# Optimization experiments

Hardware: AMD Instinct MI355X
Metric: run time of the kernel (lower is better)

## Reference

```python
import jax, jax.numpy as jnp
import numpy as np
import math

B, T1, T2, T3, D = 8, 32, 32, 16, 512
L, DL = 20, 128


def setup_inputs() -> dict:
    key = jax.random.key(0)
    ks = jax.random.split(key, 16)
    s = lambda fan: 1.0 / math.sqrt(fan)
    return {
        "f_c": jax.random.normal(ks[0], (B, T1, T2, T3, D), jnp.float32),
        "f_w": jax.random.normal(ks[1], (B, L, D), jnp.float32),
        "f_s": jax.random.normal(ks[2], (B, D), jnp.float32),
        "f_m": jax.random.normal(ks[3], (B, T1, T2, D), jnp.float32),
        "Wc_down": jax.random.normal(ks[4], (DL, D), jnp.float32) * s(D),
        "bc_down": jnp.zeros((DL,), jnp.float32),
        "Ww": jax.random.normal(ks[5], (DL, D), jnp.float32) * s(D),
        "bw": jnp.zeros((DL,), jnp.float32),
        "Ws": jax.random.normal(ks[6], (DL, D), jnp.float32) * s(D),
        "bs": jnp.zeros((DL,), jnp.float32),
        "Wq": jax.random.normal(ks[7], (DL, DL), jnp.float32) * s(DL),
        "bq": jnp.zeros((DL,), jnp.float32),
        "Wk": jax.random.normal(ks[8], (DL, DL), jnp.float32) * s(DL),
        "bk": jnp.zeros((DL,), jnp.float32),
        "Wc_up": jax.random.normal(ks[9], (D, DL), jnp.float32) * s(DL),
        "bc_up": jnp.zeros((D,), jnp.float32),
    }


def reference(f_c, f_w, f_s, f_m, Wc_down, bc_down, Ww, bw, Ws, bs,
              Wq, bq, Wk, bk, Wc_up, bc_up):
    inv_sqrt_dl = 1.0 / math.sqrt(DL)
    # 1x1 conv projections == per-position linear layers
    f_c_hat = jnp.einsum('bxyzd,ld->bxyzl', f_c, Wc_down) + bc_down  # [B,T1,T2,T3,dl]
    f_w_hat = f_w @ Ww.T + bw                                        # [B,L,dl]
    f_s_hat = f_s @ Ws.T + bs                                        # [B,dl]
    # Content attention: query from map, key/value from words
    q = f_c_hat @ Wq.T + bq                                          # [B,T1,T2,T3,dl]
    k = f_w_hat @ Wk.T + bk                                          # [B,L,dl]
    scores = jnp.einsum('bxyzd,bld->bxyzl', q, k) * inv_sqrt_dl
    attn = jax.nn.softmax(scores, axis=-1)
    f_caq = jnp.einsum('bxyzl,bld->bxyzd', attn, f_w_hat)            # [B,T1,T2,T3,dl]
    # Gate with sentence feature
    f_cq = f_c_hat * (f_caq + f_s_hat[:, None, None, None, :])
    # Self-attention over last spatial axis (T3)
    A_c = jnp.einsum('bxyzd,bxywd->bxyzw', f_cq, f_cq) * inv_sqrt_dl  # [B,T1,T2,T3,T3]
    A_c = jax.nn.softmax(A_c, axis=-1)
    f_cc_hat = jnp.einsum('bxyzw,bxywd->bxyzd', A_c, f_c_hat)
    f_cc = jnp.einsum('bxyzl,dl->bxyzd', f_cc_hat, Wc_up) + bc_up     # [B,T1,T2,T3,D]
    # Sigmoid gating residual for f_m
    g_m = jax.nn.sigmoid(f_m * f_s[:, None, None, :])
    fbar_m = g_m * f_m                                                # [B,T1,T2,D]
    return f_cc + f_c + fbar_m[:, :, :, None, :]
```

## Files before the change

### kernel.cpp

```cpp
#include <hip/hip_runtime.h>
#include <math.h>

#define B_ 8
#define T1_ 32
#define T2_ 32
#define T3_ 16
#define D_ 512
#define L_ 20
#define DL_ 128
#define M_ (B_*T1_*T2_*T3_)

#define WS_FW   0
#define WS_KQ   20480
#define WS_FS   40960
#define WS_SB   41984
#define WS_WDB  42144
#define WS_WUB  74912

typedef __attribute__((ext_vector_type(8))) short short8_t;
typedef __attribute__((ext_vector_type(4))) float f32x4;

__device__ __forceinline__ unsigned short f2b(float f) {
  unsigned int u = __float_as_uint(f);
  return (unsigned short)((u + 0x7fffu + ((u >> 16) & 1u)) >> 16);
}
__device__ __forceinline__ float b2f(short s) {
  return __uint_as_float(((unsigned)(unsigned short)s) << 16);
}
__device__ __forceinline__ int4 pack8(float4 a, float4 b) {
  int4 p;
  p.x = (int)f2b(a.x) | ((int)f2b(a.y) << 16);
  p.y = (int)f2b(a.z) | ((int)f2b(a.w) << 16);
  p.z = (int)f2b(b.x) | ((int)f2b(b.y) << 16);
  p.w = (int)f2b(b.z) | ((int)f2b(b.w) << 16);
  return p;
}

__global__ __launch_bounds__(256) void k0_convert(
    const float* __restrict__ Wd, const float* __restrict__ Wu,
    unsigned short* __restrict__ wdb, unsigned short* __restrict__ wub) {
  int g = blockIdx.x * 256 + threadIdx.x;
  if (g < 16384) {
    float4 v = ((const float4*)Wd)[g];
    ushort4 h; h.x = f2b(v.x); h.y = f2b(v.y); h.z = f2b(v.z); h.w = f2b(v.w);
    ((ushort4*)wdb)[g] = h;
  } else {
    int q = g - 16384;
    float4 v = ((const float4*)Wu)[q];
    ushort4 h; h.x = f2b(v.x); h.y = f2b(v.y); h.z = f2b(v.z); h.w = f2b(v.w);
    ((ushort4*)wub)[q] = h;
  }
}

__global__ __launch_bounds__(128) void k1_small(
    const float* __restrict__ f_w, const float* __restrict__ f_s,
    const float* __restrict__ Ww, const float* __restrict__ bw,
    const float* __restrict__ Ws, const float* __restrict__ bs,
    const float* __restrict__ Wq, const float* __restrict__ bq,
    const float* __restrict__ Wk, const float* __restrict__ bk,
    float* __restrict__ ws) {
  const int bl = blockIdx.x;
  const int b = bl / L_, l = bl % L_;
  const int d = threadIdx.x;
  __shared__ float s_fw[DL_];
  __shared__ float s_k[DL_];
  {
    const float* x = f_w + (size_t)(b*L_+l)*D_;
    const float* w = Ww + (size_t)d*D_;
    float acc = 0.f;
    for (int i = 0; i < D_; i += 4)
      acc += x[i]*w[i] + x[i+1]*w[i+1] + x[i+2]*w[i+2] + x[i+3]*w[i+3];
    acc += bw[d];
    s_fw[d] = acc;
    ws[WS_FW + (b*L_+l)*DL_ + d] = acc;
  }
  if (l == 0) {
    const float* x = f_s + (size_t)b*D_;
    const float* w = Ws + (size_t)d*D_;
    float acc = 0.f;
    for (int i = 0; i < D_; i += 4)
      acc += x[i]*w[i] + x[i+1]*w[i+1] + x[i+2]*w[i+2] + x[i+3]*w[i+3];
    ws[WS_FS + b*DL_ + d] = acc + bs[d];
  }
  __syncthreads();
  {
    const float* w = Wk + (size_t)d*DL_;
    float acc = 0.f;
    for (int i = 0; i < DL_; ++i) acc += s_fw[i]*w[i];
    s_k[d] = acc + bk[d];
  }
  __syncthreads();
  {
    float acc = 0.f;
    for (int c = 0; c < DL_; ++c) acc += s_k[c] * Wq[c*DL_ + d];
    ws[WS_KQ + (b*L_+l)*DL_ + d] = acc;
  }
  if (d == 0) {
    float acc = 0.f;
    for (int c = 0; c < DL_; ++c) acc += bq[c]*s_k[c];
    ws[WS_SB + b*L_ + l] = acc;
  }
}

#define SFCH_B 0
#define FCQ_B  8192
#define WD_B   16384
#define FC_B   32768
#define KQ_B   16384
#define FWT_B  24576
#define ATB_B  32768
#define FS_B   36864
#define SB_B   37376
#define ATTN_B 37504
#define AC_B   37504
#define WU_B   16384
#define SMEM_B 40960

__global__ __launch_bounds__(256, 4) void k2_fused(
    const float* __restrict__ f_c, const unsigned short* __restrict__ wdb,
    const unsigned short* __restrict__ wub,
    const float* __restrict__ bc_down, const float* __restrict__ bc_up,
    const float* __restrict__ f_m, const float* __restrict__ f_s,
    const float* __restrict__ ws, float* __restrict__ out) {
  __shared__ __align__(16) char smb[SMEM_B];
  float* sAttn = (float*)(smb + ATTN_B);
  float* sAc   = (float*)(smb + AC_B);
  float* sFs   = (float*)(smb + FS_B);
  float* sSb   = (float*)(smb + SB_B);

  const int t = threadIdx.x;
  const int row0 = blockIdx.x * 32;
  const int b = row0 >> 14;
  const int lane = t & 63, w = t >> 6;
  const int l15 = lane & 15, l4 = lane >> 4;
  const int wr = (w & 1) * 16;
  const int wc = w >> 1;
  const float inv_sqrt_dl = 0.08838834764831843f;
  const f32x4 z4 = {0.f, 0.f, 0.f, 0.f};
  const int sd_r = t >> 3, sd_k8 = (t & 7) * 8;

  f32x4 dacc[4];
  #pragma unroll
  for (int cf = 0; cf < 4; ++cf) dacc[cf] = z4;

  for (int kc = 0; kc < D_; kc += 64) {
    #pragma unroll
    for (int i = 0; i < 4; ++i) {
      int idx = t + i*256;
      int d = idx >> 3, kb = idx & 7;
      *(int4*)(smb + WD_B + d*128 + ((kb*16) ^ ((d & 7) << 4))) =
        *(const int4*)(wdb + (size_t)d*D_ + kc + kb*8);
    }
    {
      const float* src = f_c + (size_t)(row0 + sd_r)*D_ + kc + sd_k8;
      float4 v0 = *(const float4*)src;
      float4 v1 = *(const float4*)(src + 4);
      int4 pk = pack8(v0, v1);
      *(int4*)(smb + FC_B + sd_r*128 + ((sd_k8*2) ^ ((sd_r & 7) << 4))) = pk;
    }
    __syncthreads();
    #pragma unroll
    for (int ks = 0; ks < 2; ++ks) {
      const int rr = wr + l15;
      short8_t bfrag = *(const short8_t*)(smb + FC_B + rr*128 +
                        ((ks*64 + l4*16) ^ ((rr & 7) << 4)));
      #pragma unroll
      for (int cf = 0; cf < 4; ++cf) {
        const int d = wc*64 + cf*16 + l15;
        short8_t afrag = *(const short8_t*)(smb + WD_B + d*128 +
                          ((ks*64 + l4*16) ^ ((d & 7) << 4)));
        dacc[cf] = __builtin_amdgcn_mfma_f32_16x16x32_bf16(afrag, bfrag, dacc[cf], 0, 0, 0);
      }
    }
    __syncthreads();
  }
  {
    const int rr = wr + l15;
    const int rs = (rr & 7) << 4;
    #pragma unroll
    for (int cf = 0; cf < 4; ++cf) {
      const int d0 = wc*64 + cf*16 + l4*4;
      float4 bias = *(const float4*)(bc_down + d0);
      ushort4 pk;
      pk.x = f2b(dacc[cf][0] + bias.x); pk.y = f2b(dacc[cf][1] + bias.y);
      pk.z = f2b(dacc[cf][2] + bias.z); pk.w = f2b(dacc[cf][3] + bias.w);
      *(ushort4*)(smb + SFCH_B + rr*256 + ((d0*2) ^ rs)) = pk;
    }
  }
  for (int p = t; p < 32*16; p += 256) {
    const int l = p >> 4, k8 = (p & 15) * 8;
    int4 v = {0,0,0,0};
    if (l < L_) {
      float4 a0 = *(const float4*)(ws + WS_KQ + (b*L_+l)*DL_ + k8);
      float4 a1 = *(const float4*)(ws + WS_KQ + (b*L_+l)*DL_ + k8 + 4);
      v = pack8(a0, a1);
    }
    *(int4*)(smb + KQ_B + l*256 + ((k8*2) ^ ((l & 7) << 4))) = v;
  }
  for (int p = t; p < 512; p += 256) {
    const int d = p >> 2, l8 = (p & 3) * 8;
    float vv[8];
    #pragma unroll
    for (int e = 0; e < 8; ++e) {
      const int l = l8 + e;
      vv[e] = (l < L_) ? ws[WS_FW + (b*L_+l)*DL_ + d] : 0.f;
    }
    int4 v;
    v.x = (int)f2b(vv[0]) | ((int)f2b(vv[1]) << 16);
    v.y = (int)f2b(vv[2]) | ((int)f2b(vv[3]) << 16);
    v.z = (int)f2b(vv[4]) | ((int)f2b(vv[5]) << 16);
    v.w = (int)f2b(vv[6]) | ((int)f2b(vv[7]) << 16);
    *(int4*)(smb + FWT_B + d*64 + ((l8*2) ^ ((d & 3) << 4))) = v;
  }
  if (t < 32) *(float4*)(sFs + t*4) = *(const float4*)(ws + WS_FS + b*DL_ + t*4);
  if (t < L_) sSb[t] = ws[WS_SB + b*L_ + t];
  __syncthreads();

  {
    const int lt = w & 1, rt = w >> 1;
    const int arow = lt*16 + l15;
    const int brow = rt*16 + l15;
    f32x4 sacc = z4;
    #pragma unroll
    for (int ks = 0; ks < 4; ++ks) {
      short8_t af = *(const short8_t*)(smb + KQ_B + arow*256 +
                     ((ks*64 + l4*16) ^ ((arow & 7) << 4)));
      short8_t bf = *(const short8_t*)(smb + SFCH_B + brow*256 +
                     ((ks*64 + l4*16) ^ ((brow & 7) << 4)));
      sacc = __builtin_amdgcn_mfma_f32_16x16x32_bf16(af, bf, sacc, 0, 0, 0);
    }
    const int r2 = rt*16 + l15;
    #pragma unroll
    for (int reg = 0; reg < 4; ++reg) {
      const int lval = lt*16 + l4*4 + reg;
      if (lval < L_) sAttn[r2*21 + lval] = (sacc[reg] + sSb[lval]) * inv_sqrt_dl;
    }
  }
  __syncthreads();
  if (t < 32) {
    float* srow = sAttn + t*21;
    float m = -1e30f;
    for (int l = 0; l < L_; ++l) m = fmaxf(m, srow[l]);
    float sum = 0.f;
    for (int l = 0; l < L_; ++l) { float e = __expf(srow[l]-m); srow[l] = e; sum += e; }
    float inv = 1.f/sum;
    for (int l = 0; l < L_; ++l) srow[l] *= inv;
  }
  __syncthreads();
  {
    const int r = t >> 3, k8 = (t & 7) * 8;
    int4 v = {0,0,0,0};
    if (k8 < L_) {
      float vv[8];
      #pragma unroll
      for (int e = 0; e < 8; ++e) {
        const int l = k8 + e;
        vv[e] = (l < L_) ? sAttn[r*21 + l] : 0.f;
      }
      v.x = (int)f2b(vv[0]) | ((int)f2b(vv[1]) << 16);
      v.y = (int)f2b(vv[2]) | ((int)f2b(vv[3]) << 16);
      v.z = (int)f2b(vv[4]) | ((int)f2b(vv[5]) << 16);
      v.w = (int)f2b(vv[6]) | ((int)f2b(vv[7]) << 16);
    }
    *(int4*)(smb + ATB_B + r*128 + ((k8*2) ^ ((r & 7) << 4))) = v;
  }
  __syncthreads();
  {
    f32x4 cacc[2][2];
    cacc[0][0] = z4; cacc[0][1] = z4; cacc[1][0] = z4; cacc[1][1] = z4;
    #pragma unroll
    for (int dt = 0; dt < 2; ++dt) {
      const int arow = (w*2 + dt)*16 + l15;
      short8_t af = *(const short8_t*)(smb + FWT_B + arow*64 +
                     ((l4*16) ^ ((arow & 3) << 4)));
      #pragma unroll
      for (int rt = 0; rt < 2; ++rt) {
        const int brow = rt*16 + l15;
        short8_t bf = *(const short8_t*)(smb + ATB_B + brow*128 +
                       ((l4*16) ^ ((brow & 7) << 4)));
        cacc[dt][rt] = __builtin_amdgcn_mfma_f32_16x16x32_bf16(af, bf, cacc[dt][rt], 0, 0, 0);
      }
    }
    #pragma unroll
    for (int dt = 0; dt < 2; ++dt)
    #pragma unroll
    for (int rt = 0; rt < 2; ++rt) {
      const int d0 = (w*2 + dt)*16 + l4*4;
      const int r = rt*16 + l15;
      const int rs = (r & 7) << 4;
      float4 fs4 = *(const float4*)(sFs + d0);
      ushort4 fh = *(const ushort4*)(smb + SFCH_B + r*256 + ((d0*2) ^ rs));
      ushort4 pk;
      pk.x = f2b(b2f((short)fh.x)*(cacc[dt][rt][0] + fs4.x));
      pk.y = f2b(b2f((short)fh.y)*(cacc[dt][rt][1] + fs4.y));
      pk.z = f2b(b2f((short)fh.z)*(cacc[dt][rt][2] + fs4.z));
      pk.w = f2b(b2f((short)fh.w)*(cacc[dt][rt][3] + fs4.w));
      *(ushort4*)(smb + FCQ_B + r*256 + ((d0*2) ^ rs)) = pk;
    }
  }
  __syncthreads();
  if (w < 2) {
    const int zrow = w*16 + l15;
    f32x4 pacc = z4;
    #pragma unroll
    for (int ks = 0; ks < 4; ++ks) {
      short8_t fq = *(const short8_t*)(smb + FCQ_B + zrow*256 +
                     ((ks*64 + l4*16) ^ ((zrow & 7) << 4)));
      pacc = __builtin_amdgcn_mfma_f32_16x16x32_bf16(fq, fq, pacc, 0, 0, 0);
    }
    float p0[4], m[4], e[4], s[4];
    #pragma unroll
    for (int reg = 0; reg < 4; ++reg) p0[reg] = pacc[reg] * inv_sqrt_dl;
    #pragma unroll
    for (int reg = 0; reg < 4; ++reg) {
      m[reg] = p0[reg];
      m[reg] = fmaxf(m[reg], __shfl_xor(m[reg], 1));
      m[reg] = fmaxf(m[reg], __shfl_xor(m[reg], 2));
      m[reg] = fmaxf(m[reg], __shfl_xor(m[reg], 4));
      m[reg] = fmaxf(m[reg], __shfl_xor(m[reg], 8));
      e[reg] = __expf(p0[reg] - m[reg]);
      s[reg] = e[reg];
      s[reg] += __shfl_xor(s[reg], 1);
      s[reg] += __shfl_xor(s[reg], 2);
      s[reg] += __shfl_xor(s[reg], 4);
      s[reg] += __shfl_xor(s[reg], 8);
    }
    #pragma unroll
    for (int reg = 0; reg < 4; ++reg)
      sAc[(w*16 + l4*4 + reg)*17 + l15] = e[reg] / s[reg];
  }
  __syncthreads();
  for (int p = t; p < 1024; p += 256) {
    const int r = p >> 5, d4 = (p & 31)*4;
    const int g = r >> 4, z = r & 15;
    float ax = 0.f, ay = 0.f, az = 0.f, aw = 0.f;
    #pragma unroll
    for (int wq = 0; wq < 16; ++wq) {
      float a = sAc[(g*16+z)*17 + wq];
      const int fr = g*16 + wq;
      ushort4 fv = *(const ushort4*)(smb + SFCH_B + fr*256 + ((d4*2) ^ ((fr & 7) << 4)));
      ax += a*b2f((short)fv.x); ay += a*b2f((short)fv.y);
      az += a*b2f((short)fv.z); aw += a*b2f((short)fv.w);
    }
    ushort4 pk;
    pk.x = f2b(ax); pk.y = f2b(ay); pk.z = f2b(az); pk.w = f2b(aw);
    *(ushort4*)(smb + FCQ_B + r*256 + ((d4*2) ^ ((r & 7) << 4))) = pk;
  }
  __syncthreads();

  const int rr = wr + l15;
  const char* fcqrow = smb + FCQ_B + rr*256;
  const int xsw = (rr & 7) << 4;
  const int grow = row0 + rr;
  const size_t obase = (size_t)grow * D_;
  const size_t mbase = (size_t)(grow >> 4) * D_;
  for (int ch = 0; ch < 8; ++ch) {
    #pragma unroll
    for (int i = 0; i < 4; ++i) {
      int idx = t + i*256;
      int d = idx >> 4, kb = idx & 15;
      *(int4*)(smb + WU_B + d*256 + ((kb*16) ^ ((d & 7) << 4))) =
        *(const int4*)(wub + (size_t)(ch*64 + d)*DL_ + kb*8);
    }
    __syncthreads();
    f32x4 uacc[2]; uacc[0] = z4; uacc[1] = z4;
    #pragma unroll
    for (int ks = 0; ks < 4; ++ks) {
      short8_t bfrag = *(const short8_t*)(fcqrow + ((ks*64 + l4*16) ^ xsw));
      #pragma unroll
      for (int cf = 0; cf < 2; ++cf) {
        const int dd = wc*32 + cf*16 + l15;
        short8_t afrag = *(const short8_t*)(smb + WU_B + dd*256 +
                          ((ks*64 + l4*16) ^ ((dd & 7) << 4)));
        uacc[cf] = __builtin_amdgcn_mfma_f32_16x16x32_bf16(afrag, bfrag, uacc[cf], 0, 0, 0);
      }
    }
    #pragma unroll
    for (int cf = 0; cf < 2; ++cf) {
      const int d0 = ch*64 + wc*32 + cf*16 + l4*4;
      float4 bias = *(const float4*)(bc_up + d0);
      float4 fs4 = *(const float4*)(f_s + (size_t)b*D_ + d0);
      float4 fm4 = *(const float4*)(f_m + mbase + d0);
      float4 fc4 = *(const float4*)(f_c + obase + d0);
      float4 o;
      o.x = uacc[cf][0] + bias.x + fc4.x + fm4.x/(1.f + __expf(-fm4.x*fs4.x));
      o.y = uacc[cf][1] + bias.y + fc4.y + fm4.y/(1.f + __expf(-fm4.y*fs4.y));
      o.z = uacc[cf][2] + bias.z + fc4.z + fm4.z/(1.f + __expf(-fm4.z*fs4.z));
      o.w = uacc[cf][3] + bias.w + fc4.w + fm4.w/(1.f + __expf(-fm4.w*fs4.w));
      *(float4*)(out + obase + d0) = o;
    }
    __syncthreads();
  }
}

extern "C" void kernel_launch(void* const* d_in, const int* in_sizes, int n_in,
                              void* d_out, int out_size, void* d_ws, size_t ws_size,
                              hipStream_t stream) {
  (void)in_sizes; (void)n_in; (void)out_size; (void)ws_size;
  const float* f_c     = (const float*)d_in[0];
  const float* f_w     = (const float*)d_in[1];
  const float* f_s     = (const float*)d_in[2];
  const float* f_m     = (const float*)d_in[3];
  const float* Wc_down = (const float*)d_in[4];
  const float* bc_down = (const float*)d_in[5];
  const float* Ww      = (const float*)d_in[6];
  const float* bw      = (const float*)d_in[7];
  const float* Ws      = (const float*)d_in[8];
  const float* bs      = (const float*)d_in[9];
  const float* Wq      = (const float*)d_in[10];
  const float* bq      = (const float*)d_in[11];
  const float* Wk      = (const float*)d_in[12];
  const float* bk      = (const float*)d_in[13];
  const float* Wc_up   = (const float*)d_in[14];
  const float* bc_up   = (const float*)d_in[15];
  float* out = (float*)d_out;
  float* wsf = (float*)d_ws;
  unsigned short* wdb = (unsigned short*)(wsf + WS_WDB);
  unsigned short* wub = (unsigned short*)(wsf + WS_WUB);

  hipLaunchKernelGGL(k0_convert, dim3(128), dim3(256), 0, stream,
                     Wc_down, Wc_up, wdb, wub);
  hipLaunchKernelGGL(k1_small, dim3(B_*L_), dim3(128), 0, stream,
                     f_w, f_s, Ww, bw, Ws, bs, Wq, bq, Wk, bk, wsf);
  hipLaunchKernelGGL(k2_fused, dim3(M_/32), dim3(256), 0, stream,
                     f_c, wdb, wub, bc_down, bc_up, f_m, f_s, wsf, out);
}
```

Before: 252.9 us.

## Double-buffer weight tiles and process 64 rows per 512-thread block

Each block now handles 64 rows with 512 threads instead of 32 rows with 256, so every down- and up-projection weight tile loaded into shared memory is reused across twice as many rows. The down and up GEMM loops are software-pipelined: the next chunk's weights (and f_c) are loaded into registers during the current chunk's MFMAs and written to a second LDS buffer, which drops one barrier per iteration. The cost is shared memory growing to 80KB per block, which limits how many blocks fit per CU.

```diff
diff --git a/kernel.cpp b/kernel.cpp
--- a/kernel.cpp
+++ b/kernel.cpp
@@ -9,6 +9,7 @@
 #define L_ 20
 #define DL_ 128
 #define M_ (B_*T1_*T2_*T3_)
+#define ROWS 64
 
 #define WS_FW   0
 #define WS_KQ   20480
@@ -103,20 +104,23 @@
 }
 
 #define SFCH_B 0
-#define FCQ_B  8192
-#define WD_B   16384
-#define FC_B   32768
-#define KQ_B   16384
-#define FWT_B  24576
-#define ATB_B  32768
-#define FS_B   36864
-#define SB_B   37376
-#define ATTN_B 37504
-#define AC_B   37504
-#define WU_B   16384
-#define SMEM_B 40960
-
-__global__ __launch_bounds__(256, 4) void k2_fused(
+#define FCQ_B  16384
+#define WD0_B  32768
+#define WD1_B  49152
+#define FC0_B  65536
+#define FC1_B  73728
+#define KQ_B   32768
+#define FWT_B  40960
+#define ATB_B  49152
+#define ATTN_B 57344
+#define WU0_B  32768
+#define WU1_B  49152
+#define SB_B   76960
+#define FS_B   77056
+#define AC_B   77568
+#define SMEM_B 81920
+
+__global__ __launch_bounds__(512, 4) void k2_fused(
     const float* __restrict__ f_c, const unsigned short* __restrict__ wdb,
     const unsigned short* __restrict__ wub,
     const float* __restrict__ bc_down, const float* __restrict__ bc_up,
@@ -129,66 +133,85 @@
   float* sSb   = (float*)(smb + SB_B);
 
   const int t = threadIdx.x;
-  const int row0 = blockIdx.x * 32;
+  const int row0 = blockIdx.x * ROWS;
   const int b = row0 >> 14;
   const int lane = t & 63, w = t >> 6;
   const int l15 = lane & 15, l4 = lane >> 4;
-  const int wr = (w & 1) * 16;
-  const int wc = w >> 1;
   const float inv_sqrt_dl = 0.08838834764831843f;
   const f32x4 z4 = {0.f, 0.f, 0.f, 0.f};
-  const int sd_r = t >> 3, sd_k8 = (t & 7) * 8;
+
+  const int sd_r  = t >> 3;
+  const int sd_k8 = (t & 7) * 8;
+  const int sd_swz = (sd_k8 * 2) ^ ((sd_r & 7) << 4);
 
   f32x4 dacc[4];
   #pragma unroll
-  for (int cf = 0; cf < 4; ++cf) dacc[cf] = z4;
-
-  for (int kc = 0; kc < D_; kc += 64) {
-    #pragma unroll
-    for (int i = 0; i < 4; ++i) {
-      int idx = t + i*256;
-      int d = idx >> 3, kb = idx & 7;
-      *(int4*)(smb + WD_B + d*128 + ((kb*16) ^ ((d & 7) << 4))) =
-        *(const int4*)(wdb + (size_t)d*D_ + kc + kb*8);
-    }
-    {
-      const float* src = f_c + (size_t)(row0 + sd_r)*D_ + kc + sd_k8;
-      float4 v0 = *(const float4*)src;
-      float4 v1 = *(const float4*)(src + 4);
-      int4 pk = pack8(v0, v1);
-      *(int4*)(smb + FC_B + sd_r*128 + ((sd_k8*2) ^ ((sd_r & 7) << 4))) = pk;
-    }
-    __syncthreads();
-    #pragma unroll
-    for (int ks = 0; ks < 2; ++ks) {
-      const int rr = wr + l15;
-      short8_t bfrag = *(const short8_t*)(smb + FC_B + rr*128 +
-                        ((ks*64 + l4*16) ^ ((rr & 7) << 4)));
+  for (int rt = 0; rt < 4; ++rt) dacc[rt] = z4;
+
+  {
+    const unsigned short* wp = wdb + sd_k8;
+    int4 wrA = *(const int4*)(wp + (size_t)sd_r * D_);
+    int4 wrB = *(const int4*)(wp + (size_t)(sd_r + 64) * D_);
+    const float* src = f_c + (size_t)(row0 + sd_r) * D_ + sd_k8;
+    float4 v0 = *(const float4*)src;
+    float4 v1 = *(const float4*)(src + 4);
+    *(int4*)(smb + WD0_B + sd_r * 128 + sd_swz) = wrA;
+    *(int4*)(smb + WD0_B + (sd_r + 64) * 128 + sd_swz) = wrB;
+    *(int4*)(smb + FC0_B + sd_r * 128 + sd_swz) = pack8(v0, v1);
+  }
+  __syncthreads();
+
+  {
+    char* cur_wd = smb + WD0_B; char* nxt_wd = smb + WD1_B;
+    char* cur_fc = smb + FC0_B; char* nxt_fc = smb + FC1_B;
+    const int ad = w * 16 + l15;
+    const int aswz = (ad & 7) << 4;
+    for (int ch = 0; ch < 8; ++ch) {
+      int4 wrA, wrB; float4 v0, v1;
+      if (ch < 7) {
+        const int kn = (ch + 1) * 64;
+        const unsigned short* wp = wdb + kn + sd_k8;
+        wrA = *(const int4*)(wp + (size_t)sd_r * D_);
+        wrB = *(const int4*)(wp + (size_t)(sd_r + 64) * D_);
+        const float* src = f_c + (size_t)(row0 + sd_r) * D_ + kn + sd_k8;
+        v0 = *(const float4*)src; v1 = *(const float4*)(src + 4);
+      }
       #pragma unroll
-      for (int cf = 0; cf < 4; ++cf) {
-        const int d = wc*64 + cf*16 + l15;
-        short8_t afrag = *(const short8_t*)(smb + WD_B + d*128 +
-                          ((ks*64 + l4*16) ^ ((d & 7) << 4)));
-        dacc[cf] = __builtin_amdgcn_mfma_f32_16x16x32_bf16(afrag, bfrag, dacc[cf], 0, 0, 0);
-      }
-    }
-    __syncthreads();
-  }
-  {
-    const int rr = wr + l15;
-    const int rs = (rr & 7) << 4;
-    #pragma unroll
-    for (int cf = 0; cf < 4; ++cf) {
-      const int d0 = wc*64 + cf*16 + l4*4;
-      float4 bias = *(const float4*)(bc_down + d0);
+      for (int ks = 0; ks < 2; ++ks) {
+        short8_t afrag = *(const short8_t*)(cur_wd + ad * 128 +
+                          ((ks*64 + l4*16) ^ aswz));
+        #pragma unroll
+        for (int rt = 0; rt < 4; ++rt) {
+          const int rr = rt*16 + l15;
+          short8_t bfrag = *(const short8_t*)(cur_fc + rr * 128 +
+                            ((ks*64 + l4*16) ^ ((rr & 7) << 4)));
+          dacc[rt] = __builtin_amdgcn_mfma_f32_16x16x32_bf16(afrag, bfrag, dacc[rt], 0, 0, 0);
+        }
+      }
+      if (ch < 7) {
+        *(int4*)(nxt_wd + sd_r * 128 + sd_swz) = wrA;
+        *(int4*)(nxt_wd + (sd_r + 64) * 128 + sd_swz) = wrB;
+        *(int4*)(nxt_fc + sd_r * 128 + sd_swz) = pack8(v0, v1);
+      }
+      __syncthreads();
+      char* tw = cur_wd; cur_wd = nxt_wd; nxt_wd = tw;
+      char* tf = cur_fc; cur_fc = nxt_fc; nxt_fc = tf;
+    }
+  }
+  {
+    const int d0 = w*16 + l4*4;
+    float4 bias = *(const float4*)(bc_down + d0);
+    #pragma unroll
+    for (int rt = 0; rt < 4; ++rt) {
+      const int rr = rt*16 + l15;
       ushort4 pk;
-      pk.x = f2b(dacc[cf][0] + bias.x); pk.y = f2b(dacc[cf][1] + bias.y);
-      pk.z = f2b(dacc[cf][2] + bias.z); pk.w = f2b(dacc[cf][3] + bias.w);
-      *(ushort4*)(smb + SFCH_B + rr*256 + ((d0*2) ^ rs)) = pk;
-    }
-  }
-  for (int p = t; p < 32*16; p += 256) {
-    const int l = p >> 4, k8 = (p & 15) * 8;
+      pk.x = f2b(dacc[rt][0] + bias.x); pk.y = f2b(dacc[rt][1] + bias.y);
+      pk.z = f2b(dacc[rt][2] + bias.z); pk.w = f2b(dacc[rt][3] + bias.w);
+      *(ushort4*)(smb + SFCH_B + rr*256 + ((d0*2) ^ ((rr & 7) << 4))) = pk;
+    }
+  }
+  {
+    const int l = t >> 4, k8 = (t & 15) * 8;
     int4 v = {0,0,0,0};
     if (l < L_) {
       float4 a0 = *(const float4*)(ws + WS_KQ + (b*L_+l)*DL_ + k8);
@@ -197,8 +220,8 @@
     }
     *(int4*)(smb + KQ_B + l*256 + ((k8*2) ^ ((l & 7) << 4))) = v;
   }
-  for (int p = t; p < 512; p += 256) {
-    const int d = p >> 2, l8 = (p & 3) * 8;
+  {
+    const int d = t >> 2, l8 = (t & 3) * 8;
     float vv[8];
     #pragma unroll
     for (int e = 0; e < 8; ++e) {
@@ -217,9 +240,9 @@
   __syncthreads();
 
   {
-    const int lt = w & 1, rt = w >> 1;
+    const int lt = w & 1, rt2 = w >> 1;
     const int arow = lt*16 + l15;
-    const int brow = rt*16 + l15;
+    const int brow = rt2*16 + l15;
     f32x4 sacc = z4;
     #pragma unroll
     for (int ks = 0; ks < 4; ++ks) {
@@ -229,7 +252,7 @@
                      ((ks*64 + l4*16) ^ ((brow & 7) << 4)));
       sacc = __builtin_amdgcn_mfma_f32_16x16x32_bf16(af, bf, sacc, 0, 0, 0);
     }
-    const int r2 = rt*16 + l15;
+    const int r2 = rt2*16 + l15;
     #pragma unroll
     for (int reg = 0; reg < 4; ++reg) {
       const int lval = lt*16 + l4*4 + reg;
@@ -237,7 +260,7 @@
     }
   }
   __syncthreads();
-  if (t < 32) {
+  if (t < ROWS) {
     float* srow = sAttn + t*21;
     float m = -1e30f;
     for (int l = 0; l < L_; ++l) m = fmaxf(m, srow[l]);
@@ -266,40 +289,36 @@
   }
   __syncthreads();
   {
-    f32x4 cacc[2][2];
-    cacc[0][0] = z4; cacc[0][1] = z4; cacc[1][0] = z4; cacc[1][1] = z4;
-    #pragma unroll
-    for (int dt = 0; dt < 2; ++dt) {
-      const int arow = (w*2 + dt)*16 + l15;
-      short8_t af = *(const short8_t*)(smb + FWT_B + arow*64 +
-                     ((l4*16) ^ ((arow & 3) << 4)));
-      #pragma unroll
-      for (int rt = 0; rt < 2; ++rt) {
-        const int brow = rt*16 + l15;
-        short8_t bf = *(const short8_t*)(smb + ATB_B + brow*128 +
-                       ((l4*16) ^ ((brow & 7) << 4)));
-        cacc[dt][rt] = __builtin_amdgcn_mfma_f32_16x16x32_bf16(af, bf, cacc[dt][rt], 0, 0, 0);
-      }
-    }
-    #pragma unroll
-    for (int dt = 0; dt < 2; ++dt)
-    #pragma unroll
-    for (int rt = 0; rt < 2; ++rt) {
-      const int d0 = (w*2 + dt)*16 + l4*4;
+    f32x4 cacc[4];
+    #pragma unroll
+    for (int rt = 0; rt < 4; ++rt) cacc[rt] = z4;
+    const int arow = w*16 + l15;
+    short8_t af = *(const short8_t*)(smb + FWT_B + arow*64 +
+                   ((l4*16) ^ ((arow & 3) << 4)));
+    #pragma unroll
+    for (int rt = 0; rt < 4; ++rt) {
+      const int brow = rt*16 + l15;
+      short8_t bf = *(const short8_t*)(smb + ATB_B + brow*128 +
+                     ((l4*16) ^ ((brow & 7) << 4)));
+      cacc[rt] = __builtin_amdgcn_mfma_f32_16x16x32_bf16(af, bf, cacc[rt], 0, 0, 0);
+    }
+    const int d0 = w*16 + l4*4;
+    float4 fs4 = *(const float4*)(sFs + d0);
+    #pragma unroll
+    for (int rt = 0; rt < 4; ++rt) {
       const int r = rt*16 + l15;
       const int rs = (r & 7) << 4;
-      float4 fs4 = *(const float4*)(sFs + d0);
       ushort4 fh = *(const ushort4*)(smb + SFCH_B + r*256 + ((d0*2) ^ rs));
       ushort4 pk;
-      pk.x = f2b(b2f((short)fh.x)*(cacc[dt][rt][0] + fs4.x));
-      pk.y = f2b(b2f((short)fh.y)*(cacc[dt][rt][1] + fs4.y));
-      pk.z = f2b(b2f((short)fh.z)*(cacc[dt][rt][2] + fs4.z));
-      pk.w = f2b(b2f((short)fh.w)*(cacc[dt][rt][3] + fs4.w));
+      pk.x = f2b(b2f((short)fh.x)*(cacc[rt][0] + fs4.x));
+      pk.y = f2b(b2f((short)fh.y)*(cacc[rt][1] + fs4.y));
+      pk.z = f2b(b2f((short)fh.z)*(cacc[rt][2] + fs4.z));
+      pk.w = f2b(b2f((short)fh.w)*(cacc[rt][3] + fs4.w));
       *(ushort4*)(smb + FCQ_B + r*256 + ((d0*2) ^ rs)) = pk;
     }
   }
   __syncthreads();
-  if (w < 2) {
+  if (w < 4) {
     const int zrow = w*16 + l15;
     f32x4 pacc = z4;
     #pragma unroll
@@ -330,7 +349,17 @@
       sAc[(w*16 + l4*4 + reg)*17 + l15] = e[reg] / s[reg];
   }
   __syncthreads();
-  for (int p = t; p < 1024; p += 256) {
+
+  const int su_d = t >> 4;
+  const int su_k8 = (t & 15) * 8;
+  const int su_swz = (su_k8 * 2) ^ ((su_d & 7) << 4);
+  int4 u0, u1;
+  {
+    const unsigned short* up = wub + su_k8;
+    u0 = *(const int4*)(up + (size_t)su_d * DL_);
+    u1 = *(const int4*)(up + (size_t)(su_d + 32) * DL_);
+  }
+  for (int p = t; p < ROWS*32; p += 512) {
     const int r = p >> 5, d4 = (p & 31)*4;
     const int g = r >> 4, z = r & 15;
     float ax = 0.f, ay = 0.f, az = 0.f, aw = 0.f;
@@ -346,50 +375,59 @@
     pk.x = f2b(ax); pk.y = f2b(ay); pk.z = f2b(az); pk.w = f2b(aw);
     *(ushort4*)(smb + FCQ_B + r*256 + ((d4*2) ^ ((r & 7) << 4))) = pk;
   }
-  __syncthreads();
-
-  const int rr = wr + l15;
-  const char* fcqrow = smb + FCQ_B + rr*256;
-  const int xsw = (rr & 7) << 4;
-  const int grow = row0 + rr;
-  const size_t obase = (size_t)grow * D_;
-  const size_t mbase = (size_t)(grow >> 4) * D_;
-  for (int ch = 0; ch < 8; ++ch) {
-    #pragma unroll
-    for (int i = 0; i < 4; ++i) {
-      int idx = t + i*256;
-      int d = idx >> 4, kb = idx & 15;
-      *(int4*)(smb + WU_B + d*256 + ((kb*16) ^ ((d & 7) << 4))) =
-        *(const int4*)(wub + (size_t)(ch*64 + d)*DL_ + kb*8);
-    }
-    __syncthreads();
-    f32x4 uacc[2]; uacc[0] = z4; uacc[1] = z4;
-    #pragma unroll
-    for (int ks = 0; ks < 4; ++ks) {
-      short8_t bfrag = *(const short8_t*)(fcqrow + ((ks*64 + l4*16) ^ xsw));
+  *(int4*)(smb + WU0_B + su_d * 256 + su_swz) = u0;
+  *(int4*)(smb + WU0_B + (su_d + 32) * 256 + su_swz) = u1;
+  __syncthreads();
+
+  {
+    char* cur_wu = smb + WU0_B; char* nxt_wu = smb + WU1_B;
+    const int ad = (w & 3)*16 + l15;
+    const int aswz = (ad & 7) << 4;
+    const int rbase = (w >> 2) * 32;
+    for (int ch = 0; ch < 8; ++ch) {
+      if (ch < 7) {
+        const unsigned short* up = wub + (size_t)(ch + 1)*64*DL_ + su_k8;
+        u0 = *(const int4*)(up + (size_t)su_d * DL_);
+        u1 = *(const int4*)(up + (size_t)(su_d + 32) * DL_);
+      }
+      f32x4 uacc[2]; uacc[0] = z4; uacc[1] = z4;
       #pragma unroll
-      for (int cf = 0; cf < 2; ++cf) {
-        const int dd = wc*32 + cf*16 + l15;
-        short8_t afrag = *(const short8_t*)(smb + WU_B + dd*256 +
-                          ((ks*64 + l4*16) ^ ((dd & 7) << 4)));
-        uacc[cf] = __builtin_amdgcn_mfma_f32_16x16x32_bf16(afrag, bfrag, uacc[cf], 0, 0, 0);
-      }
-    }
-    #pragma unroll
-    for (int cf = 0; cf < 2; ++cf) {
-      const int d0 = ch*64 + wc*32 + cf*16 + l4*4;
-      float4 bias = *(const float4*)(bc_up + d0);
-      float4 fs4 = *(const float4*)(f_s + (size_t)b*D_ + d0);
-      float4 fm4 = *(const float4*)(f_m + mbase + d0);
-      float4 fc4 = *(const float4*)(f_c + obase + d0);
-      float4 o;
-      o.x = uacc[cf][0] + bias.x + fc4.x + fm4.x/(1.f + __expf(-fm4.x*fs4.x));
-      o.y = uacc[cf][1] + bias.y + fc4.y + fm4.y/(1.f + __expf(-fm4.y*fs4.y));
-      o.z = uacc[cf][2] + bias.z + fc4.z + fm4.z/(1.f + __expf(-fm4.z*fs4.z));
-      o.w = uacc[cf][3] + bias.w + fc4.w + fm4.w/(1.f + __expf(-fm4.w*fs4.w));
-      *(float4*)(out + obase + d0) = o;
-    }
-    __syncthreads();
+      for (int ks = 0; ks < 4; ++ks) {
+        short8_t afrag = *(const short8_t*)(cur_wu + ad*256 +
+                          ((ks*64 + l4*16) ^ aswz));
+        #pragma unroll
+        for (int cf = 0; cf < 2; ++cf) {
+          const int rr = rbase + cf*16 + l15;
+          short8_t bfrag = *(const short8_t*)(smb + FCQ_B + rr*256 +
+                            ((ks*64 + l4*16) ^ ((rr & 7) << 4)));
+          uacc[cf] = __builtin_amdgcn_mfma_f32_16x16x32_bf16(afrag, bfrag, uacc[cf], 0, 0, 0);
+        }
+      }
+      {
+        const int d0 = ch*64 + (w & 3)*16 + l4*4;
+        float4 bias = *(const float4*)(bc_up + d0);
+        float4 fs4 = *(const float4*)(f_s + (size_t)b*D_ + d0);
+        #pragma unroll
+        for (int cf = 0; cf < 2; ++cf) {
+          const int grow = row0 + rbase + cf*16 + l15;
+          const size_t obase = (size_t)grow * D_;
+          float4 fm4 = *(const float4*)(f_m + ((size_t)(grow >> 4))*D_ + d0);
+          float4 fc4 = *(const float4*)(f_c + obase + d0);
+          float4 o;
+          o.x = uacc[cf][0] + bias.x + fc4.x + fm4.x/(1.f + __expf(-fm4.x*fs4.x));
+          o.y = uacc[cf][1] + bias.y + fc4.y + fm4.y/(1.f + __expf(-fm4.y*fs4.y));
+          o.z = uacc[cf][2] + bias.z + fc4.z + fm4.z/(1.f + __expf(-fm4.z*fs4.z));
+          o.w = uacc[cf][3] + bias.w + fc4.w + fm4.w/(1.f + __expf(-fm4.w*fs4.w));
+          *(float4*)(out + obase + d0) = o;
+        }
+      }
+      if (ch < 7) {
+        *(int4*)(nxt_wu + su_d * 256 + su_swz) = u0;
+        *(int4*)(nxt_wu + (su_d + 32) * 256 + su_swz) = u1;
+      }
+      __syncthreads();
+      char* tu = cur_wu; cur_wu = nxt_wu; nxt_wu = tu;
+    }
   }
 }
 
@@ -422,6 +460,6 @@
                      Wc_down, Wc_up, wdb, wub);
   hipLaunchKernelGGL(k1_small, dim3(B_*L_), dim3(128), 0, stream,
                      f_w, f_s, Ww, bw, Ws, bs, Wq, bq, Wk, bk, wsf);
-  hipLaunchKernelGGL(k2_fused, dim3(M_/32), dim3(256), 0, stream,
+  hipLaunchKernelGGL(k2_fused, dim3(M_/ROWS), dim3(512), 0, stream,
                      f_c, wdb, wub, bc_down, bc_up, f_m, f_s, wsf, out);
 }
```

Measured after the change: 245.2 us. -3.1%, faster.
